# Optimization experiments

Hardware: AMD Instinct MI355X
Metric: run time of the kernel (lower is better)

## Reference

```python
import math
import jax, jax.numpy as jnp
import numpy as np

# Dims (match init_kwargs)
B, S, HID = 2, 2048, 2048
H, KVH, D = 16, 8, 128
ATTN_H = 8                      # softmax heads (head_split_dict)
TN_H = H - ATTN_H               # linear (tnorm) heads
N_REP = H // KVH                # GQA repeat factor
FIRST_TOKENS, LAST_TOKENS = 64, 512  # global prefix + band width for custom mask
EPS = 1e-6
ROPE_BASE = 1e6
SCALE = 1.0 / math.sqrt(D)


def _rope_tables(seq_len):
    inv_freq = 1.0 / (ROPE_BASE ** (jnp.arange(0, D, 2, dtype=jnp.float32) / D))
    t = jnp.arange(seq_len, dtype=jnp.float32)
    freqs = jnp.outer(t, inv_freq)                 # [S, D/2]
    emb = jnp.concatenate([freqs, freqs], axis=-1)  # [S, D]
    return jnp.cos(emb), jnp.sin(emb)


def _rotate_half(x):
    x1, x2 = jnp.split(x, 2, axis=-1)
    return jnp.concatenate([-x2, x1], axis=-1)


def _apply_rope(x, cos, sin):
    # x: [B, h, S, D], cos/sin: [S, D]
    return x * cos[None, None] + _rotate_half(x) * sin[None, None]


def _rms_norm(x):
    # SimpleRMSNorm: computed in fp32, no learned weight
    xf = x.astype(jnp.float32)
    out = xf * jax.lax.rsqrt(jnp.mean(xf * xf, axis=-1, keepdims=True) + EPS)
    return out.astype(x.dtype)


def setup_inputs() -> dict:
    key = jax.random.key(0)
    ks = jax.random.split(key, 6)
    sc = 0.02
    perm_np = np.array([3, 7, 0, 12, 9, 15, 1, 5, 2, 4, 6, 8, 10, 11, 13, 14], np.int32)
    inv_np = np.zeros(H, np.int32)
    inv_np[perm_np] = np.arange(H, dtype=np.int32)
    return {
        'hidden_states': jax.random.normal(ks[0], (B, S, HID), jnp.float32),
        'q_w': jax.random.normal(ks[1], (HID, HID), jnp.float32) * sc,
        'q_b': jnp.zeros((HID,), jnp.float32),
        'k_w': jax.random.normal(ks[2], (KVH * D, HID), jnp.float32) * sc,
        'k_b': jnp.zeros((KVH * D,), jnp.float32),
        'v_w': jax.random.normal(ks[3], (KVH * D, HID), jnp.float32) * sc,
        'v_b': jnp.zeros((KVH * D,), jnp.float32),
        'o_w': jax.random.normal(ks[4], (HID, HID), jnp.float32) * sc,
        'head_policy': jnp.array([1, 0, 1, 0, 1, 0, 1, 0], dtype=bool),
        'perm': jnp.asarray(perm_np),
        'inv_perm': jnp.asarray(inv_np),
    }


def _custom_mask(head_policy):
    # create_custom_causal_mask: banded causal + global prefix for heads with
    # policy==False; plain causal for heads with policy==True. Additive mask.
    qi = jnp.arange(S)[:, None]
    ki = jnp.arange(S)[None, :]
    causal = ki <= qi
    band = causal & ((qi - ki) < LAST_TOKENS)
    band = band | ((ki < FIRST_TOKENS) & (qi >= FIRST_TOKENS))
    neg = jnp.finfo(jnp.float32).min
    orig = jnp.where(causal, 0.0, neg)
    new = jnp.where(band, 0.0, neg)
    return jnp.where(head_policy[:, None, None], orig, new), causal  # [ATTN_H,S,S]


def reference(hidden_states, q_w, q_b, k_w, k_b, v_w, v_b, o_w,
              head_policy, perm, inv_perm):
    dt = hidden_states.dtype
    q = hidden_states @ q_w.T + q_b           # [B,S,HID]
    k = hidden_states @ k_w.T + k_b           # [B,S,KVH*D]
    v = hidden_states @ v_w.T + v_b

    # head permutation on q, then split softmax vs tnorm heads
    q = q.reshape(B, S, H, D)[:, :, perm, :]
    q = jnp.transpose(q, (0, 2, 1, 3))        # [B,H,S,D]
    kh = jnp.transpose(k.reshape(B, S, KVH, D), (0, 2, 1, 3))  # [B,KVH,S,D]
    vh = jnp.transpose(v.reshape(B, S, KVH, D), (0, 2, 1, 3))

    cos, sin = _rope_tables(S)
    q = _apply_rope(q, cos, sin)              # rope on all q heads (both branches)
    kh = _apply_rope(kh, cos, sin)

    # repeat_kv (GQA) then head permutation
    k_all = jnp.repeat(kh, N_REP, axis=1)[:, perm]  # [B,H,S,D]
    v_all = jnp.repeat(vh, N_REP, axis=1)[:, perm]

    # ---- softmax branch (first ATTN_H heads), custom banded/global mask ----
    mask, causal = _custom_mask(head_policy)
    logits = jnp.einsum('bhqd,bhkd->bhqk', q[:, :ATTN_H], k_all[:, :ATTN_H]) * SCALE
    logits = logits + mask[None]
    probs = jax.nn.softmax(logits.astype(jnp.float32), axis=-1).astype(dt)
    out_sm = jnp.einsum('bhqk,bhkd->bhqd', probs, v_all[:, :ATTN_H])
    out_sm = jnp.transpose(out_sm, (0, 2, 1, 3)).reshape(B, S, ATTN_H * D)

    # ---- linear (tnorm) branch (remaining heads): masked qk^T @ v + RMSNorm ----
    w = jnp.einsum('bhqd,bhkd->bhqk', q[:, ATTN_H:], k_all[:, ATTN_H:]) * SCALE
    w = jnp.where(causal[None, None], w, jnp.zeros((), dt))
    out_tn = jnp.einsum('bhqk,bhkd->bhqd', w, v_all[:, ATTN_H:])
    out_tn = jnp.transpose(out_tn, (0, 2, 1, 3)).reshape(B, S, TN_H * D)
    out_tn = _rms_norm(out_tn)

    # concat heads, undo permutation, output projection
    out = jnp.concatenate([out_sm, out_tn], axis=-1)
    out = out.reshape(B, S, H, D)[:, :, inv_perm, :].reshape(B, S, HID)
    return out @ o_w.T
```

## Files before the change

kernel.cpp:

```cpp
#include <hip/hip_runtime.h>
#include <hip/hip_bf16.h>
#include <stdint.h>

#define AS1 __attribute__((address_space(1)))
#define AS3 __attribute__((address_space(3)))

typedef __bf16 bf16x8 __attribute__((ext_vector_type(8)));
typedef unsigned short u16x8 __attribute__((ext_vector_type(8)));
typedef float f32x4 __attribute__((ext_vector_type(4)));

static __device__ __forceinline__ unsigned short f2bf(float f) {
  unsigned u = __float_as_uint(f);
  u += 0x7fffu + ((u >> 16) & 1u);
  return (unsigned short)(u >> 16);
}
static __device__ __forceinline__ float bf2f(unsigned short h) {
  return __uint_as_float(((unsigned)h) << 16);
}
static __device__ __forceinline__ bf16x8 ld_frag(const unsigned short* p) {
  union { u16x8 u; bf16x8 b; } c;
  c.u = *(const u16x8*)p;
  return c.b;
}
static __device__ __forceinline__ void gload16(const void* g, void* l) {
  __builtin_amdgcn_global_load_lds((AS1 const void*)g, (AS3 void*)l, 16, 0, 0);
}
#define MFMA(a, b, c) __builtin_amdgcn_mfma_f32_16x16x32_bf16(a, b, c, 0, 0, 0)

__global__ __launch_bounds__(256)
void cvt4(const float* __restrict__ in, unsigned short* __restrict__ out, long n) {
  long i = ((long)blockIdx.x * 256 + threadIdx.x) * 4;
  if (i >= n) return;
  float4 f = *(const float4*)&in[i];
  ushort4 u;
  u.x = f2bf(f.x); u.y = f2bf(f.y); u.z = f2bf(f.z); u.w = f2bf(f.w);
  *(ushort4*)&out[i] = u;
}

__global__ __launch_bounds__(256)
void rope_apply(unsigned short* __restrict__ qh, unsigned short* __restrict__ kh) {
  long i = (long)blockIdx.x * 256 + threadIdx.x;
  const long QT = (long)2 * 16 * 2048 * 64;
  unsigned short* p; long rem; float outsc;
  if (i < QT) { p = qh; rem = i; outsc = 0.08838834764831845f; }
  else        { p = kh; rem = i - QT; outsc = 1.0f; }
  int j = (int)(rem & 63);
  long row = rem >> 6;
  int s = (int)(row & 2047);
  unsigned short* x = p + row * 128;
  float inv = exp2f(-0.31143075889569023f * (float)j);
  float f = (float)s * inv;
  float sn, c;
  sincosf(f, &sn, &c);
  float x1 = bf2f(x[j]), x2 = bf2f(x[j + 64]);
  x[j]      = f2bf((x1 * c - x2 * sn) * outsc);
  x[j + 64] = f2bf((x2 * c + x1 * sn) * outsc);
}

template<int MODE>
__global__ __launch_bounds__(256, 2)
void gemm_bt(const unsigned short* __restrict__ A,
             const unsigned short* __restrict__ Bw,
             int K, int N,
             const float* __restrict__ qb, const float* __restrict__ kb,
             const float* __restrict__ vb,
             unsigned short* __restrict__ qh, unsigned short* __restrict__ kh,
             unsigned short* __restrict__ vT,
             float* __restrict__ Cout) {
  __shared__ alignas(16) unsigned short As[128 * 64];
  __shared__ alignas(16) unsigned short Bs[128 * 64];
  const int bm = blockIdx.x, bn = blockIdx.y;
  const int tid = threadIdx.x;
  const int w = tid >> 6, l = tid & 63;
  const int wm = w >> 1, wn = w & 1;
  const int l15 = l & 15, lhi = l >> 4;
  f32x4 acc[4][4] = {};
  const unsigned short* aptr = A + ((long)(bm * 128 + w * 8 + (l >> 3))) * K + (l & 7) * 8;
  const unsigned short* bptr = Bw + ((long)(bn * 128 + w * 8 + (l >> 3))) * K + (l & 7) * 8;
  unsigned short* asb = &As[w * 8 * 64];
  unsigned short* bsb = &Bs[w * 8 * 64];
  for (int k0 = 0; k0 < K; k0 += 64) {
#pragma unroll
    for (int i = 0; i < 4; ++i) {
      gload16(aptr + (long)i * 32 * K, asb + i * 2048);
      gload16(bptr + (long)i * 32 * K, bsb + i * 2048);
    }
    aptr += 64; bptr += 64;
    __syncthreads();
#pragma unroll
    for (int kk = 0; kk < 2; ++kk) {
      bf16x8 af[4], bfr[4];
#pragma unroll
      for (int m = 0; m < 4; ++m)
        af[m] = ld_frag(&As[(wm * 64 + m * 16 + l15) * 64 + kk * 32 + lhi * 8]);
#pragma unroll
      for (int n = 0; n < 4; ++n)
        bfr[n] = ld_frag(&Bs[(wn * 64 + n * 16 + l15) * 64 + kk * 32 + lhi * 8]);
#pragma unroll
      for (int m = 0; m < 4; ++m)
#pragma unroll
        for (int n = 0; n < 4; ++n)
          acc[m][n] = MFMA(af[m], bfr[n], acc[m][n]);
    }
    __syncthreads();
  }
#pragma unroll
  for (int m = 0; m < 4; ++m) {
#pragma unroll
    for (int n = 0; n < 4; ++n) {
#pragma unroll
      for (int j = 0; j < 4; ++j) {
        int row = bm * 128 + wm * 64 + m * 16 + lhi * 4 + j;
        int col = bn * 128 + wn * 64 + n * 16 + l15;
        float v = acc[m][n][j];
        if (MODE == 0) {
          int b = row >> 11, s = row & 2047;
          if (col < 2048) {
            v += qb[col];
            qh[((long)(b * 16 + (col >> 7)) * 2048 + s) * 128 + (col & 127)] = f2bf(v);
          } else if (col < 3072) {
            int c = col - 2048; v += kb[c];
            kh[((long)(b * 8 + (c >> 7)) * 2048 + s) * 128 + (c & 127)] = f2bf(v);
          } else {
            int c = col - 3072; v += vb[c];
            vT[((long)(b * 8 + (c >> 7)) * 128 + (c & 127)) * 2048 + s] = f2bf(v);
          }
        } else {
          Cout[(long)row * N + col] = v;
        }
      }
    }
  }
}

__global__ __launch_bounds__(256, 4)
void attn_all(const unsigned short* __restrict__ qheads,
              const unsigned short* __restrict__ kheads,
              const unsigned short* __restrict__ vT,
              unsigned short* __restrict__ aout,
              unsigned short* __restrict__ tnb,
              const int* __restrict__ perm) {
  __shared__ alignas(16) unsigned short Ks[64 * 128];
  __shared__ alignas(16) unsigned short Vs[128 * 64];
  __shared__ alignas(16) unsigned short Ps[4][16 * 64];
  const int q0 = blockIdx.x * 64;
  const int hy = blockIdx.y;
  const int b = blockIdx.z;
  const bool sm = hy < 8;
  const bool banded = sm && ((hy & 1) != 0);
  const int qhd = perm[hy];
  const int kvh = qhd >> 1;
  const int tid = threadIdx.x, w = tid >> 6, l = tid & 63, l15 = l & 15, lhi = l >> 4;
  const unsigned short* Qg = qheads + ((long)(b * 16 + qhd) * 2048 + q0) * 128;
  const unsigned short* Kg = kheads + (long)(b * 8 + kvh) * 2048 * 128;
  const unsigned short* Vg = vT + (long)(b * 8 + kvh) * 128 * 2048;
  bf16x8 qf[4];
#pragma unroll
  for (int c = 0; c < 4; ++c)
    qf[c] = ld_frag(Qg + (w * 16 + l15) * 128 + c * 32 + lhi * 8);
  f32x4 ao[8] = {};
  float lsum[4] = {0.f, 0.f, 0.f, 0.f};
  const int krow = w * 4 + (l >> 4);
  const long kgoff = (long)krow * 128 + (((l & 15) * 8) ^ ((krow & 7) << 3));
  unsigned short* kdst = &Ks[w * 512];
  const int vrow = w * 8 + (l >> 3);
  const long vgoff = (long)vrow * 2048 + (((l & 7) * 8) ^ ((vrow & 7) << 3));
  unsigned short* vdst = &Vs[w * 512];
  const int rsw15 = (l15 & 7) << 3;

  for (int k0 = 0; k0 <= q0; k0 += 64) {
    if (banded && k0 >= 64 && q0 - k0 >= 575) continue;
    __syncthreads();
#pragma unroll
    for (int p = 0; p < 4; ++p)
      gload16(Kg + (long)(k0 + p * 16) * 128 + kgoff, kdst + p * 2048);
#pragma unroll
    for (int p = 0; p < 4; ++p)
      gload16(Vg + (long)p * 32 * 2048 + k0 + vgoff, vdst + p * 2048);
    __syncthreads();
    f32x4 sacc[4] = {};
#pragma unroll
    for (int c = 0; c < 4; ++c) {
#pragma unroll
      for (int ks = 0; ks < 4; ++ks) {
        bf16x8 kf = ld_frag(&Ks[(ks * 16 + l15) * 128 + ((c * 32 + lhi * 8) ^ rsw15)]);
        sacc[ks] = MFMA(qf[c], kf, sacc[ks]);
      }
    }
    const int qrb = q0 + w * 16 + lhi * 4;
#pragma unroll
    for (int j = 0; j < 4; ++j) {
      const int q = qrb + j;
      const int prow = lhi * 4 + j;
      const int psw = (prow & 7) << 3;
#pragma unroll
      for (int ks = 0; ks < 4; ++ks) {
        int k = k0 + ks * 16 + l15;
        bool ok = (k <= q) && (!banded || k < 64 || (q - k) < 512);
        float p;
        if (sm) { p = ok ? __expf(sacc[ks][j]) : 0.f; lsum[j] += p; }
        else    { p = ok ? sacc[ks][j] : 0.f; }
        Ps[w][prow * 64 + ((ks * 16 + l15) ^ psw)] = f2bf(p);
      }
    }
    bf16x8 pa0 = ld_frag(&Ps[w][l15 * 64 + ((lhi * 8) ^ rsw15)]);
    bf16x8 pa1 = ld_frag(&Ps[w][l15 * 64 + ((32 + lhi * 8) ^ rsw15)]);
#pragma unroll
    for (int n = 0; n < 8; ++n) {
      bf16x8 vf0 = ld_frag(&Vs[(n * 16 + l15) * 64 + ((lhi * 8) ^ rsw15)]);
      bf16x8 vf1 = ld_frag(&Vs[(n * 16 + l15) * 64 + ((32 + lhi * 8) ^ rsw15)]);
      ao[n] = MFMA(pa0, vf0, ao[n]);
      ao[n] = MFMA(pa1, vf1, ao[n]);
    }
  }
  if (sm) {
#pragma unroll
    for (int j = 0; j < 4; ++j) {
      float s = lsum[j];
#pragma unroll
      for (int d = 1; d < 16; d <<= 1) s += __shfl_xor(s, d);
      float inv = 1.0f / s;
      int q = q0 + w * 16 + lhi * 4 + j;
      unsigned short* o = aout + ((long)b * 2048 + q) * 2048 + qhd * 128;
#pragma unroll
      for (int n = 0; n < 8; ++n) o[n * 16 + l15] = f2bf(ao[n][j] * inv);
    }
  } else {
    const int hidx = hy - 8;
#pragma unroll
    for (int j = 0; j < 4; ++j) {
      int q = q0 + w * 16 + lhi * 4 + j;
      unsigned short* o = tnb + ((long)b * 2048 + q) * 1024 + hidx * 128;
#pragma unroll
      for (int n = 0; n < 8; ++n) o[n * 16 + l15] = f2bf(ao[n][j]);
    }
  }
}

__global__ __launch_bounds__(256)
void rms_scatter(const unsigned short* __restrict__ tnb,
                 unsigned short* __restrict__ aout,
                 const int* __restrict__ perm) {
  __shared__ float wsum[4];
  int row = blockIdx.x, tid = threadIdx.x;
  const unsigned short* x = tnb + (long)row * 1024;
  ushort4 u = *(const ushort4*)&x[tid * 4];
  float v0 = bf2f(u.x), v1 = bf2f(u.y), v2 = bf2f(u.z), v3 = bf2f(u.w);
  float ss = v0 * v0 + v1 * v1 + v2 * v2 + v3 * v3;
#pragma unroll
  for (int d = 1; d < 64; d <<= 1) ss += __shfl_xor(ss, d);
  if ((tid & 63) == 0) wsum[tid >> 6] = ss;
  __syncthreads();
  float tot = wsum[0] + wsum[1] + wsum[2] + wsum[3];
  float r = rsqrtf(tot * (1.0f / 1024.0f) + 1e-6f);
  int slot = perm[8 + (tid >> 5)];
  unsigned short* o = aout + (long)row * 2048 + slot * 128 + ((tid * 4) & 127);
  o[0] = f2bf(v0 * r); o[1] = f2bf(v1 * r); o[2] = f2bf(v2 * r); o[3] = f2bf(v3 * r);
}

extern "C" void kernel_launch(void* const* d_in, const int* in_sizes, int n_in,
                              void* d_out, int out_size, void* d_ws, size_t ws_size,
                              hipStream_t stream) {
  const float* hs  = (const float*)d_in[0];
  const float* q_w = (const float*)d_in[1];
  const float* q_b = (const float*)d_in[2];
  const float* k_w = (const float*)d_in[3];
  const float* k_b = (const float*)d_in[4];
  const float* v_w = (const float*)d_in[5];
  const float* v_b = (const float*)d_in[6];
  const float* o_w = (const float*)d_in[7];
  const int* perm  = (const int*)d_in[9];

  char* ws = (char*)d_ws;
  unsigned short* hbf  = (unsigned short*)(ws + 0);
  unsigned short* wqkv = (unsigned short*)(ws + 16777216);
  unsigned short* kh   = (unsigned short*)(ws + 33554432);
  unsigned short* vT   = (unsigned short*)(ws + 41943040);
  unsigned short* qh   = (unsigned short*)d_out;
  unsigned short* aout = hbf;
  unsigned short* tnb  = wqkv;
  unsigned short* owb  = kh;
  float* outF = (float*)d_out;

  cvt4<<<8192, 256, 0, stream>>>(hs, hbf, 8388608);
  cvt4<<<4096, 256, 0, stream>>>(q_w, wqkv, 4194304);
  cvt4<<<2048, 256, 0, stream>>>(k_w, wqkv + 4194304, 2097152);
  cvt4<<<2048, 256, 0, stream>>>(v_w, wqkv + 6291456, 2097152);
  gemm_bt<0><<<dim3(32, 32), 256, 0, stream>>>(hbf, wqkv, 2048, 4096,
                                               q_b, k_b, v_b, qh, kh, vT, nullptr);
  rope_apply<<<24576, 256, 0, stream>>>(qh, kh);
  attn_all<<<dim3(32, 16, 2), 256, 0, stream>>>(qh, kh, vT, aout, tnb, perm);
  cvt4<<<4096, 256, 0, stream>>>(o_w, owb, 4194304);
  rms_scatter<<<4096, 256, 0, stream>>>(tnb, aout, perm);
  gemm_bt<1><<<dim3(32, 16), 256, 0, stream>>>(aout, owb, 2048, 2048,
                                               nullptr, nullptr, nullptr,
                                               nullptr, nullptr, nullptr, outF);
}
```

Baseline: 316.8 us.

## Replace QKV projection GEMM with 256x256 double-buffered swizzled 8-wave kernel

The QKV projection moves from a 128x128-tile single-buffered GEMM to a dedicated 256x256-tile kernel with 512 threads. It double-buffers LDS with staggered global-to-LDS prefetch, XOR-swizzles LDS to avoid bank conflicts, raises wave priority around MFMA bursts, and remaps block IDs for better L2 locality. The goal is higher arithmetic intensity and overlap of loads with MFMA on the largest GEMM. The cost is 128KB of LDS per block and many barriers, which limits occupancy. The output-projection GEMM is only simplified.

```diff
diff --git a/kernel.cpp b/kernel.cpp
--- a/kernel.cpp
+++ b/kernel.cpp
@@ -26,6 +26,8 @@
   __builtin_amdgcn_global_load_lds((AS1 const void*)g, (AS3 void*)l, 16, 0, 0);
 }
 #define MFMA(a, b, c) __builtin_amdgcn_mfma_f32_16x16x32_bf16(a, b, c, 0, 0, 0)
+#define BAR asm volatile("s_barrier" ::: "memory")
+#define VM4 asm volatile("s_waitcnt vmcnt(4)" ::: "memory")
 
 __global__ __launch_bounds__(256)
 void cvt4(const float* __restrict__ in, unsigned short* __restrict__ out, long n) {
@@ -57,16 +59,126 @@
   x[j + 64] = f2bf((x2 * c + x1 * sn) * outsc);
 }
 
-template<int MODE>
+__global__ __launch_bounds__(512, 2)
+void gemm256_qkv(const unsigned short* __restrict__ A,
+                 const unsigned short* __restrict__ Bw,
+                 const float* __restrict__ qb, const float* __restrict__ kb,
+                 const float* __restrict__ vb,
+                 unsigned short* __restrict__ qh, unsigned short* __restrict__ kh,
+                 unsigned short* __restrict__ vT) {
+  constexpr int K = 2048, NT = K / 64, NIT = NT / 2;
+  __shared__ alignas(16) unsigned short LDS[65536];
+  const int id = blockIdx.x;
+  const int lg = (id & 7) * 32 + (id >> 3);
+  const int bm = lg >> 4, bn = lg & 15;
+  const int tid = threadIdx.x;
+  const int wid = tid >> 6, lane = tid & 63;
+  const int wr = wid >> 2, wc = wid & 3;
+  const int l15 = lane & 15, lhi = lane >> 4;
+  const int rsw = (l15 & 7) << 3;
+  const int srow0 = wid * 8 + (lane >> 3);
+  const int scol = ((lane & 7) ^ (lane >> 3)) * 8;
+  const unsigned short* Ag = A + (long)(bm * 256) * K;
+  const unsigned short* Bg = Bw + (long)(bn * 256) * K;
+  unsigned short* Al = LDS;
+  unsigned short* Bl = LDS + 32768;
+
+#define STG(gb, lb, p, h, t) do {                                              \
+    int tc = (t) < NT ? (t) : NT - 1;                                          \
+    gload16((gb) + (long)((h) * 128 + srow0) * K + tc * 64 + scol,             \
+            (lb) + (p) * 16384 + (h) * 8192 + wid * 512);                      \
+    gload16((gb) + (long)((h) * 128 + 64 + srow0) * K + tc * 64 + scol,        \
+            (lb) + (p) * 16384 + (h) * 8192 + 4096 + wid * 512);               \
+  } while (0)
+
+#define LDA(p, mh) do {                                                        \
+    _Pragma("unroll") for (int m4 = 0; m4 < 4; ++m4)                           \
+    _Pragma("unroll") for (int kk = 0; kk < 2; ++kk)                           \
+      afr[m4][kk] = ld_frag(&Al[(p) * 16384 +                                  \
+          (wr * 128 + (mh) * 64 + m4 * 16 + l15) * 64 +                        \
+          ((kk * 32 + lhi * 8) ^ rsw)]);                                       \
+  } while (0)
+
+#define LDB(p, nh) do {                                                        \
+    _Pragma("unroll") for (int n2 = 0; n2 < 2; ++n2)                           \
+    _Pragma("unroll") for (int kk = 0; kk < 2; ++kk)                           \
+      bfr[nh][n2][kk] = ld_frag(&Bl[(p) * 16384 +                              \
+          (wc * 64 + (nh) * 32 + n2 * 16 + l15) * 64 +                         \
+          ((kk * 32 + lhi * 8) ^ rsw)]);                                       \
+  } while (0)
+
+#define QUAD(mh, nh) do {                                                      \
+    __builtin_amdgcn_s_setprio(1);                                             \
+    _Pragma("unroll") for (int m4 = 0; m4 < 4; ++m4)                           \
+    _Pragma("unroll") for (int n2 = 0; n2 < 2; ++n2)                           \
+    _Pragma("unroll") for (int kk = 0; kk < 2; ++kk)                           \
+      acc[(mh) * 4 + m4][(nh) * 2 + n2] =                                      \
+          MFMA(afr[m4][kk], bfr[nh][n2][kk], acc[(mh) * 4 + m4][(nh) * 2 + n2]);\
+    __builtin_amdgcn_s_setprio(0);                                             \
+  } while (0)
+
+  f32x4 acc[8][4] = {};
+  bf16x8 afr[4][2], bfr[2][2][2];
+
+  STG(Bg, Bl, 0, 0, 0); STG(Bg, Bl, 0, 1, 0);
+  STG(Ag, Al, 0, 0, 0); STG(Ag, Al, 0, 1, 0);
+  STG(Bg, Bl, 1, 0, 1); STG(Bg, Bl, 1, 1, 1);
+  VM4; BAR;
+
+  for (int it = 0; it < NIT; ++it) {
+    const int T = 2 * it;
+    LDA(0, 0); LDB(0, 0); STG(Ag, Al, 1, 0, T + 1);
+    BAR; QUAD(0, 0); BAR;
+    LDB(0, 1);            STG(Ag, Al, 1, 1, T + 1);
+    BAR; QUAD(0, 1); BAR;
+    LDA(0, 1);            STG(Bg, Bl, 0, 0, T + 2);
+    BAR; QUAD(1, 0); BAR;
+                          STG(Bg, Bl, 0, 1, T + 2);
+    VM4; BAR; QUAD(1, 1); BAR;
+    LDA(1, 0); LDB(1, 0); STG(Ag, Al, 0, 0, T + 2);
+    BAR; QUAD(0, 0); BAR;
+    LDB(1, 1);            STG(Ag, Al, 0, 1, T + 2);
+    BAR; QUAD(0, 1); BAR;
+    LDA(1, 1);            STG(Bg, Bl, 1, 0, T + 3);
+    BAR; QUAD(1, 0); BAR;
+                          STG(Bg, Bl, 1, 1, T + 3);
+    VM4; BAR; QUAD(1, 1); BAR;
+  }
+
+  const int r0 = bm * 256 + wr * 128, c0 = bn * 256 + wc * 64;
+#pragma unroll
+  for (int m = 0; m < 8; ++m) {
+#pragma unroll
+    for (int n = 0; n < 4; ++n) {
+#pragma unroll
+      for (int j = 0; j < 4; ++j) {
+        int row = r0 + m * 16 + lhi * 4 + j;
+        int col = c0 + n * 16 + l15;
+        float v = acc[m][n][j];
+        int b = row >> 11, s = row & 2047;
+        if (col < 2048) {
+          v += qb[col];
+          qh[((long)(b * 16 + (col >> 7)) * 2048 + s) * 128 + (col & 127)] = f2bf(v);
+        } else if (col < 3072) {
+          int c = col - 2048; v += kb[c];
+          kh[((long)(b * 8 + (c >> 7)) * 2048 + s) * 128 + (c & 127)] = f2bf(v);
+        } else {
+          int c = col - 3072; v += vb[c];
+          vT[((long)(b * 8 + (c >> 7)) * 128 + (c & 127)) * 2048 + s] = f2bf(v);
+        }
+      }
+    }
+  }
+#undef STG
+#undef LDA
+#undef LDB
+#undef QUAD
+}
+
 __global__ __launch_bounds__(256, 2)
 void gemm_bt(const unsigned short* __restrict__ A,
              const unsigned short* __restrict__ Bw,
-             int K, int N,
-             const float* __restrict__ qb, const float* __restrict__ kb,
-             const float* __restrict__ vb,
-             unsigned short* __restrict__ qh, unsigned short* __restrict__ kh,
-             unsigned short* __restrict__ vT,
-             float* __restrict__ Cout) {
+             int K, int N, float* __restrict__ Cout) {
   __shared__ alignas(16) unsigned short As[128 * 64];
   __shared__ alignas(16) unsigned short Bs[128 * 64];
   const int bm = blockIdx.x, bn = blockIdx.y;
@@ -105,32 +217,15 @@
     __syncthreads();
   }
 #pragma unroll
-  for (int m = 0; m < 4; ++m) {
-#pragma unroll
-    for (int n = 0; n < 4; ++n) {
+  for (int m = 0; m < 4; ++m)
+#pragma unroll
+    for (int n = 0; n < 4; ++n)
 #pragma unroll
       for (int j = 0; j < 4; ++j) {
         int row = bm * 128 + wm * 64 + m * 16 + lhi * 4 + j;
         int col = bn * 128 + wn * 64 + n * 16 + l15;
-        float v = acc[m][n][j];
-        if (MODE == 0) {
-          int b = row >> 11, s = row & 2047;
-          if (col < 2048) {
-            v += qb[col];
-            qh[((long)(b * 16 + (col >> 7)) * 2048 + s) * 128 + (col & 127)] = f2bf(v);
-          } else if (col < 3072) {
-            int c = col - 2048; v += kb[c];
-            kh[((long)(b * 8 + (c >> 7)) * 2048 + s) * 128 + (c & 127)] = f2bf(v);
-          } else {
-            int c = col - 3072; v += vb[c];
-            vT[((long)(b * 8 + (c >> 7)) * 128 + (c & 127)) * 2048 + s] = f2bf(v);
-          }
-        } else {
-          Cout[(long)row * N + col] = v;
-        }
+        Cout[(long)row * N + col] = acc[m][n][j];
       }
-    }
-  }
 }
 
 __global__ __launch_bounds__(256, 4)
@@ -286,13 +381,10 @@
   cvt4<<<4096, 256, 0, stream>>>(q_w, wqkv, 4194304);
   cvt4<<<2048, 256, 0, stream>>>(k_w, wqkv + 4194304, 2097152);
   cvt4<<<2048, 256, 0, stream>>>(v_w, wqkv + 6291456, 2097152);
-  gemm_bt<0><<<dim3(32, 32), 256, 0, stream>>>(hbf, wqkv, 2048, 4096,
-                                               q_b, k_b, v_b, qh, kh, vT, nullptr);
+  gemm256_qkv<<<256, 512, 0, stream>>>(hbf, wqkv, q_b, k_b, v_b, qh, kh, vT);
   rope_apply<<<24576, 256, 0, stream>>>(qh, kh);
   attn_all<<<dim3(32, 16, 2), 256, 0, stream>>>(qh, kh, vT, aout, tnb, perm);
   cvt4<<<4096, 256, 0, stream>>>(o_w, owb, 4194304);
   rms_scatter<<<4096, 256, 0, stream>>>(tnb, aout, perm);
-  gemm_bt<1><<<dim3(32, 16), 256, 0, stream>>>(aout, owb, 2048, 2048,
-                                               nullptr, nullptr, nullptr,
-                                               nullptr, nullptr, nullptr, outF);
-}
+  gemm_bt<<<dim3(32, 16), 256, 0, stream>>>(aout, owb, 2048, 2048, outF);
+}
```

Result: faster. 285.6 us (-9.8%).
